# Optimization experiments

Hardware: AMD Instinct MI355X
Metric: run time of the kernel (lower is better)

Reference implementation:

```python
import jax, jax.numpy as jnp
import numpy as np

WIN = 64
SHIFT = 32
HEADS = 12


def setup_inputs() -> dict:
    key = jax.random.key(0)
    ks = jax.random.split(key, 6)
    D = 768
    return {
        'x': jax.random.normal(ks[0], (16, 4096, D), dtype=jnp.float32),
        'qkv_w': jax.random.normal(ks[1], (3 * D, D), dtype=jnp.float32) * (D ** -0.5),
        'qkv_b': jax.random.normal(ks[2], (3 * D,), dtype=jnp.float32) * 0.02,
        'proj_w': jax.random.normal(ks[3], (D, D), dtype=jnp.float32) * (D ** -0.5),
        'proj_b': jax.random.normal(ks[4], (D,), dtype=jnp.float32) * 0.02,
        'rel_bias': jax.random.normal(ks[5], (HEADS, 2 * WIN - 1), dtype=jnp.float32) * 0.02,
    }


def reference(x, qkv_w, qkv_b, proj_w, proj_b, rel_bias):
    B, N, D = x.shape
    H, hd = HEADS, D // HEADS
    scale = hd ** -0.5
    if SHIFT:
        x = jnp.roll(x, SHIFT, axis=1)
    pad = (-N) % WIN
    if pad:
        x = jnp.pad(x, ((0, 0), (0, pad), (0, 0)))
    Np = x.shape[1]
    nW = Np // WIN
    # [B*nW, w, D] windows
    xw = x.reshape(B * nW, WIN, D)
    qkv = xw @ qkv_w.T + qkv_b                       # [B*nW, w, 3D]
    qkv = qkv.reshape(B * nW, WIN, 3, H, hd).transpose(2, 0, 3, 1, 4)
    q, k, v = qkv[0], qkv[1], qkv[2]                 # [B*nW, H, w, hd]
    attn = jnp.einsum('bhqd,bhkd->bhqk', q, k) * scale
    idx = jnp.arange(WIN)
    rel = idx[None, :] - idx[:, None] + (WIN - 1)    # [w, w] in [0, 2w-2]
    attn = attn + rel_bias[:, rel][None]             # gather bias per head
    attn = jax.nn.softmax(attn, axis=-1)
    y = jnp.einsum('bhqk,bhkd->bhqd', attn, v)       # [B*nW, H, w, hd]
    y = y.transpose(0, 2, 1, 3).reshape(B * nW, WIN, D)
    y = y @ proj_w.T + proj_b
    y = y.reshape(B, Np, D)
    if pad:
        y = y[:, :N, :]
    if SHIFT:
        y = jnp.roll(y, -SHIFT, axis=1)
    return y
```

## Files before the change

kernel.cpp:

```cpp
#include <hip/hip_runtime.h>
#include <hip/hip_bf16.h>
#include <stdint.h>

#define SEQ     4096
#define NBATCH  16
#define DMODEL  768
#define NHEAD   12
#define HDIM    64
#define WINSZ   64
#define SHIFT_T 32
#define QKV_N   (3*DMODEL)

typedef __attribute__((ext_vector_type(8)))  short bf16x8;
typedef __attribute__((ext_vector_type(4)))  float f32x4;

static __device__ __forceinline__ unsigned short f2bf(float f) {
  union { float f; unsigned u; } v; v.f = f;
  unsigned r = v.u + 0x7fffu + ((v.u >> 16) & 1u);
  return (unsigned short)(r >> 16);
}

#define G2L(gp, lp) __builtin_amdgcn_global_load_lds( \
    (const __attribute__((address_space(1))) unsigned*)(const void*)(gp), \
    (__attribute__((address_space(3))) unsigned*)(void*)(lp), 16, 0, 0)

__global__ void k_cvt_x(const float* __restrict__ x, unsigned short* __restrict__ xb,
                        long long c0, long long n8) {
  for (long long i = (long long)blockIdx.x*blockDim.x + threadIdx.x; i < n8;
       i += (long long)gridDim.x*blockDim.x) {
    long long e = i*8;
    int d = (int)(e % DMODEL);
    long long gt = c0 + e / DMODEL;
    int t = (int)(gt & (SEQ-1));
    long long b = gt >> 12;
    int ts = (t - SHIFT_T) & (SEQ-1);
    const float* src = x + (((b << 12) + ts) * (long long)DMODEL + d);
    float4 a0 = *(const float4*)src;
    float4 a1 = *(const float4*)(src + 4);
    bf16x8 o;
    o[0]=(short)f2bf(a0.x); o[1]=(short)f2bf(a0.y); o[2]=(short)f2bf(a0.z); o[3]=(short)f2bf(a0.w);
    o[4]=(short)f2bf(a1.x); o[5]=(short)f2bf(a1.y); o[6]=(short)f2bf(a1.z); o[7]=(short)f2bf(a1.w);
    *(bf16x8*)(xb + e) = o;
  }
}

__global__ void k_cvt_w(const float* __restrict__ w, unsigned short* __restrict__ wb, int n8) {
  int i = blockIdx.x*blockDim.x + threadIdx.x;
  if (i >= n8) return;
  float4 a0 = ((const float4*)w)[2*i];
  float4 a1 = ((const float4*)w)[2*i+1];
  bf16x8 o;
  o[0]=(short)f2bf(a0.x); o[1]=(short)f2bf(a0.y); o[2]=(short)f2bf(a0.z); o[3]=(short)f2bf(a0.w);
  o[4]=(short)f2bf(a1.x); o[5]=(short)f2bf(a1.y); o[6]=(short)f2bf(a1.z); o[7]=(short)f2bf(a1.w);
  ((bf16x8*)wb)[i] = o;
}

#define MFMA16(a,b,c) __builtin_amdgcn_mfma_f32_16x16x32_bf16(a,b,c,0,0,0)
#define LDS8(p) (*(const bf16x8*)(p))

template<int MODE>
__global__ __launch_bounds__(512, 1)
void k_gemm256(const unsigned short* __restrict__ A, const unsigned short* __restrict__ Bw,
               const float* __restrict__ bias, unsigned short* __restrict__ Cb,
               float* __restrict__ Cf, int M, int N, int K, int nTN, long long c0) {
  __shared__ char lds[131072];
  const int nt = K >> 6;
  int nwg = gridDim.x;
  int cpx = nwg >> 3;
  int wg  = (blockIdx.x & 7) * cpx + (blockIdx.x >> 3);
  int bm = wg / nTN, bn = wg - bm*nTN;
  long long m0 = (long long)bm * 256;
  int n0 = bn * 256;
  int tid = threadIdx.x;
  int lane = tid & 63, wid = tid >> 6;
  int wr = wid >> 2, wc = wid & 3;
  int cl = lane & 15, g4 = lane >> 4;

  const long long K2 = 2LL * K;
  int L  = tid * 16;
  int Ls = L ^ (((L >> 7) & 7) << 4);
  int srow = Ls >> 7, scol = Ls & 127;
  const char* gAr0 = (const char*)A + (m0 +       srow) * K2 + scol;
  const char* gAr1 = (const char*)A + (m0 +  64 + srow) * K2 + scol;
  const char* gAr2 = (const char*)A + (m0 + 128 + srow) * K2 + scol;
  const char* gAr3 = (const char*)A + (m0 + 192 + srow) * K2 + scol;
  const char* gBr0 = (const char*)Bw + (long long)(n0 +       srow) * K2 + scol;
  const char* gBr1 = (const char*)Bw + (long long)(n0 +  64 + srow) * K2 + scol;
  const char* gBr2 = (const char*)Bw + (long long)(n0 + 128 + srow) * K2 + scol;
  const char* gBr3 = (const char*)Bw + (long long)(n0 + 192 + srow) * K2 + scol;

  int p0 = cl*128 + ((g4*16) ^ ((cl & 7) << 4));
  int p1 = p0 ^ 64;
  int RA0 = wr*16384;
  int RA1 = wr*16384 + 8192;
  int BB  = 32768 + wc*8192;

  f32x4 acc[8][4];
  #pragma unroll
  for (int i = 0; i < 8; ++i)
    #pragma unroll
    for (int j = 0; j < 4; ++j) acc[i][j] = (f32x4){0.f,0.f,0.f,0.f};

#define MMPH(MA, MB, x0, x1, y0, y1) \
  acc[MA][0]=MFMA16(x0,b00,acc[MA][0]); acc[MA][1]=MFMA16(x0,b10,acc[MA][1]); \
  acc[MA][2]=MFMA16(x0,b20,acc[MA][2]); acc[MA][3]=MFMA16(x0,b30,acc[MA][3]); \
  acc[MB][0]=MFMA16(y0,b00,acc[MB][0]); acc[MB][1]=MFMA16(y0,b10,acc[MB][1]); \
  acc[MB][2]=MFMA16(y0,b20,acc[MB][2]); acc[MB][3]=MFMA16(y0,b30,acc[MB][3]); \
  acc[MA][0]=MFMA16(x1,b01,acc[MA][0]); acc[MA][1]=MFMA16(x1,b11,acc[MA][1]); \
  acc[MA][2]=MFMA16(x1,b21,acc[MA][2]); acc[MA][3]=MFMA16(x1,b31,acc[MA][3]); \
  acc[MB][0]=MFMA16(y1,b01,acc[MB][0]); acc[MB][1]=MFMA16(y1,b11,acc[MB][1]); \
  acc[MB][2]=MFMA16(y1,b21,acc[MB][2]); acc[MB][3]=MFMA16(y1,b31,acc[MB][3]);

#define BARR __builtin_amdgcn_s_barrier()
#define SBAR __builtin_amdgcn_sched_barrier(0)
#define LGK0 do { asm volatile("s_waitcnt lgkmcnt(0)" ::: "memory"); SBAR; } while(0)

#define TILE(RD, ST, DOSTAGE, WBSTR, DOWA) do {                               \
    const char* rb = (RD); char* stb = (ST);                                  \
    bf16x8 b00,b01,b10,b11,b20,b21,b30,b31;                                   \
    {                              \
      bf16x8 x0 = LDS8(rb + RA0        + p0), x1 = LDS8(rb + RA0        + p1);\
      bf16x8 y0 = LDS8(rb + RA0 + 2048 + p0), y1 = LDS8(rb + RA0 + 2048 + p1);\
      b00 = LDS8(rb + BB        + p0);  b01 = LDS8(rb + BB        + p1);      \
      b10 = LDS8(rb + BB + 2048 + p0);  b11 = LDS8(rb + BB + 2048 + p1);      \
      b20 = LDS8(rb + BB + 4096 + p0);  b21 = LDS8(rb + BB + 4096 + p1);      \
      b30 = LDS8(rb + BB + 6144 + p0);  b31 = LDS8(rb + BB + 6144 + p1);      \
      if (DOSTAGE) { G2L(gBr0, stb + 32768 + L); G2L(gBr1, stb + 40960 + L); }\
      asm volatile("s_waitcnt lgkmcnt(8)" ::: "memory"); SBAR;                \
      BARR; LGK0;                                                             \
      __builtin_amdgcn_s_setprio(1);                                          \
      MMPH(0, 1, x0, x1, y0, y1)                                              \
      __builtin_amdgcn_s_setprio(0); SBAR; BARR;                              \
    }                                                                         \
    {              \
      bf16x8 x0 = LDS8(rb + RA0 + 4096 + p0), x1 = LDS8(rb + RA0 + 4096 + p1);\
      bf16x8 y0 = LDS8(rb + RA0 + 6144 + p0), y1 = LDS8(rb + RA0 + 6144 + p1);\
      if (DOSTAGE) { G2L(gBr2, stb + 49152 + L); G2L(gBr3, stb + 57344 + L); }\
      SBAR; BARR; LGK0;                                                       \
      __builtin_amdgcn_s_setprio(1);                                          \
      MMPH(2, 3, x0, x1, y0, y1)                                              \
      __builtin_amdgcn_s_setprio(0); SBAR;                                    \
      asm volatile(WBSTR ::: "memory"); SBAR; BARR;                           \
    }                                                                         \
    {                                      \
      bf16x8 x0 = LDS8(rb + RA1        + p0), x1 = LDS8(rb + RA1        + p1);\
      bf16x8 y0 = LDS8(rb + RA1 + 2048 + p0), y1 = LDS8(rb + RA1 + 2048 + p1);\
      if (DOSTAGE) { G2L(gAr0, stb + L); G2L(gAr2, stb + 16384 + L); }        \
      SBAR; BARR; LGK0;                                                       \
      __builtin_amdgcn_s_setprio(1);                                          \
      MMPH(4, 5, x0, x1, y0, y1)                                              \
      __builtin_amdgcn_s_setprio(0); SBAR; BARR;                              \
    }                                                                         \
    {        \
      bf16x8 x0 = LDS8(rb + RA1 + 4096 + p0), x1 = LDS8(rb + RA1 + 4096 + p1);\
      bf16x8 y0 = LDS8(rb + RA1 + 6144 + p0), y1 = LDS8(rb + RA1 + 6144 + p1);\
      if (DOSTAGE) { G2L(gAr1, stb + 8192 + L); G2L(gAr3, stb + 24576 + L);   \
                     gAr0 += 128; gAr1 += 128; gAr2 += 128; gAr3 += 128;      \
                     gBr0 += 128; gBr1 += 128; gBr2 += 128; gBr3 += 128; }    \
      SBAR; BARR; LGK0;                                                       \
      __builtin_amdgcn_s_setprio(1);                                          \
      MMPH(6, 7, x0, x1, y0, y1)                                              \
      __builtin_amdgcn_s_setprio(0); SBAR;                                    \
      if (DOWA) { asm volatile("s_waitcnt vmcnt(2)" ::: "memory"); }          \
      SBAR; BARR;                                                             \
    }                                                                         \
  } while (0)

  G2L(gBr0, lds + 32768 + L); G2L(gBr1, lds + 40960 + L);
  G2L(gBr2, lds + 49152 + L); G2L(gBr3, lds + 57344 + L);
  G2L(gAr0, lds + L);         G2L(gAr2, lds + 16384 + L);
  G2L(gAr1, lds + 8192 + L);  G2L(gAr3, lds + 24576 + L);
  gAr0 += 128; gAr1 += 128; gAr2 += 128; gAr3 += 128;
  gBr0 += 128; gBr1 += 128; gBr2 += 128; gBr3 += 128;
  asm volatile("s_waitcnt vmcnt(2)" ::: "memory");
  SBAR; BARR;

  char* const bufA = lds;
  char* const bufB = lds + 65536;
  for (int i = 0; i < (nt - 2) / 2; ++i) {
    TILE(bufA, bufB, 1, "s_waitcnt vmcnt(4)", 1);
    TILE(bufB, bufA, 1, "s_waitcnt vmcnt(4)", 1);
  }
  TILE(bufA, bufB, 1, "s_waitcnt vmcnt(4)", 1);
  TILE(bufB, bufA, 0, "s_waitcnt vmcnt(0)", 0);
#undef TILE
#undef MMPH

  #pragma unroll
  for (int mf = 0; mf < 8; ++mf) {
    #pragma unroll
    for (int nf = 0; nf < 4; ++nf) {
      int n = n0 + wc*64 + nf*16 + cl;
      float bv = bias[n];
      #pragma unroll
      for (int r = 0; r < 4; ++r) {
        long long m = m0 + wr*128 + mf*16 + g4*4 + r;
        float v = acc[mf][nf][r] + bv;
        if (MODE == 0) {
          Cb[m * (long long)N + n] = f2bf(v);
        } else {
          long long gm = c0 + m;
          long long om = (gm & ~(long long)(SEQ-1)) | ((gm - SHIFT_T) & (long long)(SEQ-1));
          Cf[om * (long long)N + n] = v;
        }
      }
    }
  }
}

__global__ __launch_bounds__(256, 4)
void k_attn(const unsigned short* __restrict__ qkv, const float* __restrict__ rel_bias,
            unsigned short* __restrict__ y) {
  int w = blockIdx.x / NHEAD;
  int h = blockIdx.x - w*NHEAD;
  __shared__ unsigned short sQ[64*72], sK[64*72], sV[64*72];
  __shared__ unsigned short sP[4][16*72];
  __shared__ float rb[128];
  int tid = threadIdx.x, lane = tid & 63, wid = tid >> 6;
  int cl = lane & 15, g4 = lane >> 4;

  if (tid < 2*WINSZ - 1) rb[tid] = rel_bias[h*(2*WINSZ-1) + tid];

  const unsigned short* base = qkv + (long long)w*WINSZ*QKV_N + h*HDIM;
  #pragma unroll
  for (int pass = 0; pass < 2; ++pass) {
    int row = (tid >> 3) + pass*32;
    int ch  = tid & 7;
    const unsigned short* src = base + (long long)row*QKV_N + ch*8;
    *(bf16x8*)(sQ + row*72 + ch*8) = *(const bf16x8*)(src);
    *(bf16x8*)(sK + row*72 + ch*8) = *(const bf16x8*)(src + DMODEL);
    *(bf16x8*)(sV + row*72 + ch*8) = *(const bf16x8*)(src + 2*DMODEL);
  }
  __syncthreads();

  f32x4 sc[4];
  #pragma unroll
  for (int nt = 0; nt < 4; ++nt) sc[nt] = (f32x4){0.f,0.f,0.f,0.f};
  #pragma unroll
  for (int kk = 0; kk < 2; ++kk) {
    bf16x8 aq = *(const bf16x8*)(sQ + (wid*16 + cl)*72 + kk*32 + g4*8);
    #pragma unroll
    for (int nt = 0; nt < 4; ++nt) {
      bf16x8 bk = *(const bf16x8*)(sK + (nt*16 + cl)*72 + kk*32 + g4*8);
      sc[nt] = __builtin_amdgcn_mfma_f32_16x16x32_bf16(aq, bk, sc[nt], 0, 0, 0);
    }
  }

  float pv[4][4];
  #pragma unroll
  for (int r = 0; r < 4; ++r) {
    int qi = wid*16 + g4*4 + r;
    float mx = -1e30f;
    #pragma unroll
    for (int nt = 0; nt < 4; ++nt) {
      int kj = nt*16 + cl;
      float v = sc[nt][r]*0.125f + rb[kj - qi + (WINSZ-1)];
      pv[nt][r] = v;
      mx = fmaxf(mx, v);
    }
    #pragma unroll
    for (int m = 1; m < 16; m <<= 1) mx = fmaxf(mx, __shfl_xor(mx, m, 64));
    float sum = 0.f;
    #pragma unroll
    for (int nt = 0; nt < 4; ++nt) { float e = __expf(pv[nt][r]-mx); pv[nt][r] = e; sum += e; }
    #pragma unroll
    for (int m = 1; m < 16; m <<= 1) sum += __shfl_xor(sum, m, 64);
    float inv = 1.f / sum;
    #pragma unroll
    for (int nt = 0; nt < 4; ++nt)
      sP[wid][(g4*4+r)*72 + nt*16 + cl] = f2bf(pv[nt][r]*inv);
  }

  f32x4 o[4];
  #pragma unroll
  for (int nt = 0; nt < 4; ++nt) o[nt] = (f32x4){0.f,0.f,0.f,0.f};
  #pragma unroll
  for (int kk = 0; kk < 2; ++kk) {
    bf16x8 ap = *(const bf16x8*)(&sP[wid][cl*72 + kk*32 + g4*8]);
    #pragma unroll
    for (int nt = 0; nt < 4; ++nt) {
      bf16x8 bv;
      #pragma unroll
      for (int j = 0; j < 8; ++j)
        bv[j] = (short)sV[(kk*32 + g4*8 + j)*72 + nt*16 + cl];
      o[nt] = __builtin_amdgcn_mfma_f32_16x16x32_bf16(ap, bv, o[nt], 0, 0, 0);
    }
  }

  long long tokbase = (long long)w * WINSZ;
  #pragma unroll
  for (int nt = 0; nt < 4; ++nt)
    #pragma unroll
    for (int r = 0; r < 4; ++r) {
      int row = wid*16 + g4*4 + r;
      y[(tokbase + row) * (long long)DMODEL + h*HDIM + nt*16 + cl] = f2bf(o[nt][r]);
    }
}

extern "C" void kernel_launch(void* const* d_in, const int* in_sizes, int n_in,
                              void* d_out, int out_size, void* d_ws, size_t ws_size,
                              hipStream_t stream) {
  const float* x      = (const float*)d_in[0];
  const float* qkv_w  = (const float*)d_in[1];
  const float* qkv_b  = (const float*)d_in[2];
  const float* proj_w = (const float*)d_in[3];
  const float* proj_b = (const float*)d_in[4];
  const float* rel_b  = (const float*)d_in[5];
  float* out = (float*)d_out;

  const long long NTOK = (long long)NBATCH * SEQ;
  const size_t wbytes = (size_t)QKV_N*DMODEL*2 + (size_t)DMODEL*DMODEL*2;

  int C = 16;
  for (int c : {1, 2, 4, 8, 16}) {
    size_t tpc = (size_t)NTOK / c;
    size_t need = tpc*QKV_N*2 + tpc*DMODEL*2 + wbytes;
    if (need <= ws_size) { C = c; break; }
  }
  long long tpc = NTOK / C;

  char* ws = (char*)d_ws;
  unsigned short* qkvb = (unsigned short*)ws;
  unsigned short* xb   = (unsigned short*)(ws + (size_t)tpc*QKV_N*2);
  unsigned short* wq   = (unsigned short*)(ws + (size_t)tpc*QKV_N*2 + (size_t)tpc*DMODEL*2);
  unsigned short* wp   = wq + (size_t)QKV_N*DMODEL;

  k_cvt_w<<<(QKV_N*DMODEL/8 + 255)/256, 256, 0, stream>>>(qkv_w, wq, QKV_N*DMODEL/8);
  k_cvt_w<<<(DMODEL*DMODEL/8 + 255)/256, 256, 0, stream>>>(proj_w, wp, DMODEL*DMODEL/8);

  for (int c = 0; c < C; ++c) {
    long long c0 = (long long)c * tpc;
    long long n8 = tpc * DMODEL / 8;
    int cvtGrid = (int)((n8 + 255) / 256); if (cvtGrid > 2048) cvtGrid = 2048;
    k_cvt_x<<<cvtGrid, 256, 0, stream>>>(x, xb, c0, n8);

    int mT = (int)(tpc / 256);
    k_gemm256<0><<<mT * (QKV_N/256), 512, 0, stream>>>(xb, wq, qkv_b, qkvb, nullptr,
                                                       (int)tpc, QKV_N, DMODEL, QKV_N/256, c0);
    k_attn<<<(int)(tpc/WINSZ) * NHEAD, 256, 0, stream>>>(qkvb, rel_b, xb );
    k_gemm256<1><<<mT * (DMODEL/256), 512, 0, stream>>>(xb, wp, proj_b, nullptr, out,
                                                        (int)tpc, DMODEL, DMODEL, DMODEL/256, c0);
  }
}
```

Measured before the change: 503.3 us.

## Fuse x conversion, QKV projection and window attention into one kernel

```diff
diff --git a/kernel.cpp b/kernel.cpp
--- a/kernel.cpp
+++ b/kernel.cpp
@@ -24,25 +24,8 @@
     (const __attribute__((address_space(1))) unsigned*)(const void*)(gp), \
     (__attribute__((address_space(3))) unsigned*)(void*)(lp), 16, 0, 0)
 
-__global__ void k_cvt_x(const float* __restrict__ x, unsigned short* __restrict__ xb,
-                        long long c0, long long n8) {
-  for (long long i = (long long)blockIdx.x*blockDim.x + threadIdx.x; i < n8;
-       i += (long long)gridDim.x*blockDim.x) {
-    long long e = i*8;
-    int d = (int)(e % DMODEL);
-    long long gt = c0 + e / DMODEL;
-    int t = (int)(gt & (SEQ-1));
-    long long b = gt >> 12;
-    int ts = (t - SHIFT_T) & (SEQ-1);
-    const float* src = x + (((b << 12) + ts) * (long long)DMODEL + d);
-    float4 a0 = *(const float4*)src;
-    float4 a1 = *(const float4*)(src + 4);
-    bf16x8 o;
-    o[0]=(short)f2bf(a0.x); o[1]=(short)f2bf(a0.y); o[2]=(short)f2bf(a0.z); o[3]=(short)f2bf(a0.w);
-    o[4]=(short)f2bf(a1.x); o[5]=(short)f2bf(a1.y); o[6]=(short)f2bf(a1.z); o[7]=(short)f2bf(a1.w);
-    *(bf16x8*)(xb + e) = o;
-  }
-}
+#define MFMA16(a,b,c) __builtin_amdgcn_mfma_f32_16x16x32_bf16(a,b,c,0,0,0)
+#define LDS8(p) (*(const bf16x8*)(p))
 
 __global__ void k_cvt_w(const float* __restrict__ w, unsigned short* __restrict__ wb, int n8) {
   int i = blockIdx.x*blockDim.x + threadIdx.x;
@@ -55,8 +38,177 @@
   ((bf16x8*)wb)[i] = o;
 }
 
-#define MFMA16(a,b,c) __builtin_amdgcn_mfma_f32_16x16x32_bf16(a,b,c,0,0,0)
-#define LDS8(p) (*(const bf16x8*)(p))
+__global__ __launch_bounds__(512, 4)
+void k_qkv_attn(const float* __restrict__ x, const unsigned short* __restrict__ wqkv,
+                const float* __restrict__ qkv_b, const float* __restrict__ rel_bias,
+                unsigned short* __restrict__ y) {
+  __shared__ char ldsA[16384];
+  __shared__ char ldsS[55296];
+  __shared__ float rb[128];
+  int blk = blockIdx.x;
+  int tid = threadIdx.x, lane = tid & 63, wid = tid >> 6;
+  int cl = lane & 15, g4 = lane >> 4;
+  int wr = wid >> 2, wc = wid & 3;
+
+  int arow = tid >> 2, ac4 = tid & 3;
+  long long gt = (long long)blk*128 + arow;
+  long long bb = gt >> 12;
+  int ts = ((int)(gt & (SEQ-1)) - SHIFT_T) & (SEQ-1);
+  const float* xsrc = x + ((bb << 12) + ts) * (long long)DMODEL + ac4*16;
+  int akey = (arow & 7) << 4;
+  int awb0 = arow*128 + ((ac4*32)      ^ akey);
+  int awb1 = arow*128 + ((ac4*32 + 16) ^ akey);
+
+  int L  = tid * 16;
+  int Ls = L ^ (((L >> 7) & 7) << 4);
+  int srow = Ls >> 7, scol = Ls & 127;
+
+  int key = (cl & 7) << 4;
+  int am  = (wr*64 + cl) * 128;
+  int ch0 = (g4*16) ^ key;
+  int ch1 = ch0 ^ 64;
+  int bn  = (wc*16 + cl) * 128;
+
+  const long long BROW = 2LL * DMODEL;
+  unsigned short* sQKV = (unsigned short*)ldsS;
+
+  for (int h = 0; h < NHEAD; ++h) {
+    const char* gB0 = (const char*)wqkv + (h*64 + srow) * BROW + scol;
+    const char* gB1 = gB0 + 768 * BROW;
+    const char* gB2 = gB1 + 768 * BROW;
+
+    f32x4 acc[4][3];
+    #pragma unroll
+    for (int i = 0; i < 4; ++i)
+      #pragma unroll
+      for (int j = 0; j < 3; ++j) acc[i][j] = (f32x4){0.f,0.f,0.f,0.f};
+
+    for (int kt = 0; kt < 12; ++kt) {
+      __syncthreads();
+      const float* xs = xsrc + kt*64;
+      float4 f0 = *(const float4*)xs;
+      float4 f1 = *(const float4*)(xs + 4);
+      float4 f2 = *(const float4*)(xs + 8);
+      float4 f3 = *(const float4*)(xs + 12);
+      bf16x8 v0, v1;
+      v0[0]=(short)f2bf(f0.x); v0[1]=(short)f2bf(f0.y); v0[2]=(short)f2bf(f0.z); v0[3]=(short)f2bf(f0.w);
+      v0[4]=(short)f2bf(f1.x); v0[5]=(short)f2bf(f1.y); v0[6]=(short)f2bf(f1.z); v0[7]=(short)f2bf(f1.w);
+      v1[0]=(short)f2bf(f2.x); v1[1]=(short)f2bf(f2.y); v1[2]=(short)f2bf(f2.z); v1[3]=(short)f2bf(f2.w);
+      v1[4]=(short)f2bf(f3.x); v1[5]=(short)f2bf(f3.y); v1[6]=(short)f2bf(f3.z); v1[7]=(short)f2bf(f3.w);
+      *(bf16x8*)(ldsA + awb0) = v0;
+      *(bf16x8*)(ldsA + awb1) = v1;
+      G2L(gB0 + kt*128, ldsS + L);
+      G2L(gB1 + kt*128, ldsS + 8192 + L);
+      G2L(gB2 + kt*128, ldsS + 16384 + L);
+      __syncthreads();
+      bf16x8 a0[4], a1[4], b0[3], b1[3];
+      #pragma unroll
+      for (int mr = 0; mr < 4; ++mr) {
+        a0[mr] = LDS8(ldsA + am + mr*2048 + ch0);
+        a1[mr] = LDS8(ldsA + am + mr*2048 + ch1);
+      }
+      #pragma unroll
+      for (int nf = 0; nf < 3; ++nf) {
+        b0[nf] = LDS8(ldsS + nf*8192 + bn + ch0);
+        b1[nf] = LDS8(ldsS + nf*8192 + bn + ch1);
+      }
+      #pragma unroll
+      for (int mr = 0; mr < 4; ++mr)
+        #pragma unroll
+        for (int nf = 0; nf < 3; ++nf) {
+          acc[mr][nf] = MFMA16(a0[mr], b0[nf], acc[mr][nf]);
+          acc[mr][nf] = MFMA16(a1[mr], b1[nf], acc[mr][nf]);
+        }
+    }
+    __syncthreads();
+    #pragma unroll
+    for (int nf = 0; nf < 3; ++nf) {
+      float bv = qkv_b[nf*768 + h*64 + wc*16 + cl];
+      #pragma unroll
+      for (int mr = 0; mr < 4; ++mr)
+        #pragma unroll
+        for (int r = 0; r < 4; ++r) {
+          int row = wr*64 + mr*16 + g4*4 + r;
+          sQKV[nf*9216 + row*72 + wc*16 + cl] = f2bf(acc[mr][nf][r] + bv);
+        }
+    }
+    if (tid < 2*WINSZ - 1) rb[tid] = rel_bias[h*(2*WINSZ-1) + tid];
+    __syncthreads();
+
+    {
+      int wl = wid >> 2, ww = wid & 3;
+      unsigned short* sQ = sQKV +          wl*64*72;
+      unsigned short* sK = sQKV +  9216 + wl*64*72;
+      unsigned short* sV = sQKV + 18432 + wl*64*72;
+      char* sPb = ldsA + wid*2048;
+
+      f32x4 sc[4];
+      #pragma unroll
+      for (int nt = 0; nt < 4; ++nt) sc[nt] = (f32x4){0.f,0.f,0.f,0.f};
+      #pragma unroll
+      for (int kk = 0; kk < 2; ++kk) {
+        bf16x8 aq = LDS8(sQ + (ww*16 + cl)*72 + kk*32 + g4*8);
+        #pragma unroll
+        for (int nt = 0; nt < 4; ++nt) {
+          bf16x8 bk = LDS8(sK + (nt*16 + cl)*72 + kk*32 + g4*8);
+          sc[nt] = MFMA16(aq, bk, sc[nt]);
+        }
+      }
+
+      float pv[4][4];
+      #pragma unroll
+      for (int r = 0; r < 4; ++r) {
+        int qi = ww*16 + g4*4 + r;
+        float mx = -1e30f;
+        #pragma unroll
+        for (int nt = 0; nt < 4; ++nt) {
+          int kj = nt*16 + cl;
+          float v = sc[nt][r]*0.125f + rb[kj - qi + (WINSZ-1)];
+          pv[nt][r] = v;
+          mx = fmaxf(mx, v);
+        }
+        #pragma unroll
+        for (int m = 1; m < 16; m <<= 1) mx = fmaxf(mx, __shfl_xor(mx, m, 64));
+        float sum = 0.f;
+        #pragma unroll
+        for (int nt = 0; nt < 4; ++nt) { float e = __expf(pv[nt][r]-mx); pv[nt][r] = e; sum += e; }
+        #pragma unroll
+        for (int m = 1; m < 16; m <<= 1) sum += __shfl_xor(sum, m, 64);
+        float inv = 1.f / sum;
+        int prow = g4*4 + r;
+        int pkey = (prow & 7) << 4;
+        #pragma unroll
+        for (int nt = 0; nt < 4; ++nt)
+          *(unsigned short*)(sPb + prow*128 + (((nt*16 + cl)*2) ^ pkey)) = f2bf(pv[nt][r]*inv);
+      }
+
+      f32x4 o[4];
+      #pragma unroll
+      for (int nt = 0; nt < 4; ++nt) o[nt] = (f32x4){0.f,0.f,0.f,0.f};
+      #pragma unroll
+      for (int kk = 0; kk < 2; ++kk) {
+        bf16x8 ap = LDS8(sPb + cl*128 + ((kk*64 + g4*16) ^ ((cl & 7) << 4)));
+        #pragma unroll
+        for (int nt = 0; nt < 4; ++nt) {
+          bf16x8 bv;
+          #pragma unroll
+          for (int j = 0; j < 8; ++j)
+            bv[j] = (short)sV[(kk*32 + g4*8 + j)*72 + nt*16 + cl];
+          o[nt] = MFMA16(ap, bv, o[nt]);
+        }
+      }
+
+      long long tokbase = (long long)blk * 128;
+      #pragma unroll
+      for (int nt = 0; nt < 4; ++nt)
+        #pragma unroll
+        for (int r = 0; r < 4; ++r) {
+          int row = wid*16 + g4*4 + r;
+          y[(tokbase + row) * (long long)DMODEL + h*HDIM + nt*16 + cl] = f2bf(o[nt][r]);
+        }
+    }
+  }
+}
 
 template<int MODE>
 __global__ __launch_bounds__(512, 1)
@@ -116,15 +268,15 @@
 #define LGK0 do { asm volatile("s_waitcnt lgkmcnt(0)" ::: "memory"); SBAR; } while(0)
 
 #define TILE(RD, ST, DOSTAGE, WBSTR, DOWA) do {                               \
-    const char* rb = (RD); char* stb = (ST);                                  \
+    const char* rbuf = (RD); char* stb = (ST);                                \
     bf16x8 b00,b01,b10,b11,b20,b21,b30,b31;                                   \
-    {                              \
-      bf16x8 x0 = LDS8(rb + RA0        + p0), x1 = LDS8(rb + RA0        + p1);\
-      bf16x8 y0 = LDS8(rb + RA0 + 2048 + p0), y1 = LDS8(rb + RA0 + 2048 + p1);\
-      b00 = LDS8(rb + BB        + p0);  b01 = LDS8(rb + BB        + p1);      \
-      b10 = LDS8(rb + BB + 2048 + p0);  b11 = LDS8(rb + BB + 2048 + p1);      \
-      b20 = LDS8(rb + BB + 4096 + p0);  b21 = LDS8(rb + BB + 4096 + p1);      \
-      b30 = LDS8(rb + BB + 6144 + p0);  b31 = LDS8(rb + BB + 6144 + p1);      \
+    {                                                            \
+      bf16x8 x0 = LDS8(rbuf + RA0        + p0), x1 = LDS8(rbuf + RA0        + p1);\
+      bf16x8 y0 = LDS8(rbuf + RA0 + 2048 + p0), y1 = LDS8(rbuf + RA0 + 2048 + p1);\
+      b00 = LDS8(rbuf + BB        + p0);  b01 = LDS8(rbuf + BB        + p1);  \
+      b10 = LDS8(rbuf + BB + 2048 + p0);  b11 = LDS8(rbuf + BB + 2048 + p1);  \
+      b20 = LDS8(rbuf + BB + 4096 + p0);  b21 = LDS8(rbuf + BB + 4096 + p1);  \
+      b30 = LDS8(rbuf + BB + 6144 + p0);  b31 = LDS8(rbuf + BB + 6144 + p1);  \
       if (DOSTAGE) { G2L(gBr0, stb + 32768 + L); G2L(gBr1, stb + 40960 + L); }\
       asm volatile("s_waitcnt lgkmcnt(8)" ::: "memory"); SBAR;                \
       BARR; LGK0;                                                             \
@@ -132,9 +284,9 @@
       MMPH(0, 1, x0, x1, y0, y1)                                              \
       __builtin_amdgcn_s_setprio(0); SBAR; BARR;                              \
     }                                                                         \
-    {              \
-      bf16x8 x0 = LDS8(rb + RA0 + 4096 + p0), x1 = LDS8(rb + RA0 + 4096 + p1);\
-      bf16x8 y0 = LDS8(rb + RA0 + 6144 + p0), y1 = LDS8(rb + RA0 + 6144 + p1);\
+    {                                                            \
+      bf16x8 x0 = LDS8(rbuf + RA0 + 4096 + p0), x1 = LDS8(rbuf + RA0 + 4096 + p1);\
+      bf16x8 y0 = LDS8(rbuf + RA0 + 6144 + p0), y1 = LDS8(rbuf + RA0 + 6144 + p1);\
       if (DOSTAGE) { G2L(gBr2, stb + 49152 + L); G2L(gBr3, stb + 57344 + L); }\
       SBAR; BARR; LGK0;                                                       \
       __builtin_amdgcn_s_setprio(1);                                          \
@@ -142,18 +294,18 @@
       __builtin_amdgcn_s_setprio(0); SBAR;                                    \
       asm volatile(WBSTR ::: "memory"); SBAR; BARR;                           \
     }                                                                         \
-    {                                      \
-      bf16x8 x0 = LDS8(rb + RA1        + p0), x1 = LDS8(rb + RA1        + p1);\
-      bf16x8 y0 = LDS8(rb + RA1 + 2048 + p0), y1 = LDS8(rb + RA1 + 2048 + p1);\
+    {                                                            \
+      bf16x8 x0 = LDS8(rbuf + RA1        + p0), x1 = LDS8(rbuf + RA1        + p1);\
+      bf16x8 y0 = LDS8(rbuf + RA1 + 2048 + p0), y1 = LDS8(rbuf + RA1 + 2048 + p1);\
       if (DOSTAGE) { G2L(gAr0, stb + L); G2L(gAr2, stb + 16384 + L); }        \
       SBAR; BARR; LGK0;                                                       \
       __builtin_amdgcn_s_setprio(1);                                          \
       MMPH(4, 5, x0, x1, y0, y1)                                              \
       __builtin_amdgcn_s_setprio(0); SBAR; BARR;                              \
     }                                                                         \
-    {        \
-      bf16x8 x0 = LDS8(rb + RA1 + 4096 + p0), x1 = LDS8(rb + RA1 + 4096 + p1);\
-      bf16x8 y0 = LDS8(rb + RA1 + 6144 + p0), y1 = LDS8(rb + RA1 + 6144 + p1);\
+    {                                                            \
+      bf16x8 x0 = LDS8(rbuf + RA1 + 4096 + p0), x1 = LDS8(rbuf + RA1 + 4096 + p1);\
+      bf16x8 y0 = LDS8(rbuf + RA1 + 6144 + p0), y1 = LDS8(rbuf + RA1 + 6144 + p1);\
       if (DOSTAGE) { G2L(gAr1, stb + 8192 + L); G2L(gAr3, stb + 24576 + L);   \
                      gAr0 += 128; gAr1 += 128; gAr2 += 128; gAr3 += 128;      \
                      gBr0 += 128; gBr1 += 128; gBr2 += 128; gBr3 += 128; }    \
@@ -208,95 +360,6 @@
   }
 }
 
-__global__ __launch_bounds__(256, 4)
-void k_attn(const unsigned short* __restrict__ qkv, const float* __restrict__ rel_bias,
-            unsigned short* __restrict__ y) {
-  int w = blockIdx.x / NHEAD;
-  int h = blockIdx.x - w*NHEAD;
-  __shared__ unsigned short sQ[64*72], sK[64*72], sV[64*72];
-  __shared__ unsigned short sP[4][16*72];
-  __shared__ float rb[128];
-  int tid = threadIdx.x, lane = tid & 63, wid = tid >> 6;
-  int cl = lane & 15, g4 = lane >> 4;
-
-  if (tid < 2*WINSZ - 1) rb[tid] = rel_bias[h*(2*WINSZ-1) + tid];
-
-  const unsigned short* base = qkv + (long long)w*WINSZ*QKV_N + h*HDIM;
-  #pragma unroll
-  for (int pass = 0; pass < 2; ++pass) {
-    int row = (tid >> 3) + pass*32;
-    int ch  = tid & 7;
-    const unsigned short* src = base + (long long)row*QKV_N + ch*8;
-    *(bf16x8*)(sQ + row*72 + ch*8) = *(const bf16x8*)(src);
-    *(bf16x8*)(sK + row*72 + ch*8) = *(const bf16x8*)(src + DMODEL);
-    *(bf16x8*)(sV + row*72 + ch*8) = *(const bf16x8*)(src + 2*DMODEL);
-  }
-  __syncthreads();
-
-  f32x4 sc[4];
-  #pragma unroll
-  for (int nt = 0; nt < 4; ++nt) sc[nt] = (f32x4){0.f,0.f,0.f,0.f};
-  #pragma unroll
-  for (int kk = 0; kk < 2; ++kk) {
-    bf16x8 aq = *(const bf16x8*)(sQ + (wid*16 + cl)*72 + kk*32 + g4*8);
-    #pragma unroll
-    for (int nt = 0; nt < 4; ++nt) {
-      bf16x8 bk = *(const bf16x8*)(sK + (nt*16 + cl)*72 + kk*32 + g4*8);
-      sc[nt] = __builtin_amdgcn_mfma_f32_16x16x32_bf16(aq, bk, sc[nt], 0, 0, 0);
-    }
-  }
-
-  float pv[4][4];
-  #pragma unroll
-  for (int r = 0; r < 4; ++r) {
-    int qi = wid*16 + g4*4 + r;
-    float mx = -1e30f;
-    #pragma unroll
-    for (int nt = 0; nt < 4; ++nt) {
-      int kj = nt*16 + cl;
-      float v = sc[nt][r]*0.125f + rb[kj - qi + (WINSZ-1)];
-      pv[nt][r] = v;
-      mx = fmaxf(mx, v);
-    }
-    #pragma unroll
-    for (int m = 1; m < 16; m <<= 1) mx = fmaxf(mx, __shfl_xor(mx, m, 64));
-    float sum = 0.f;
-    #pragma unroll
-    for (int nt = 0; nt < 4; ++nt) { float e = __expf(pv[nt][r]-mx); pv[nt][r] = e; sum += e; }
-    #pragma unroll
-    for (int m = 1; m < 16; m <<= 1) sum += __shfl_xor(sum, m, 64);
-    float inv = 1.f / sum;
-    #pragma unroll
-    for (int nt = 0; nt < 4; ++nt)
-      sP[wid][(g4*4+r)*72 + nt*16 + cl] = f2bf(pv[nt][r]*inv);
-  }
-
-  f32x4 o[4];
-  #pragma unroll
-  for (int nt = 0; nt < 4; ++nt) o[nt] = (f32x4){0.f,0.f,0.f,0.f};
-  #pragma unroll
-  for (int kk = 0; kk < 2; ++kk) {
-    bf16x8 ap = *(const bf16x8*)(&sP[wid][cl*72 + kk*32 + g4*8]);
-    #pragma unroll
-    for (int nt = 0; nt < 4; ++nt) {
-      bf16x8 bv;
-      #pragma unroll
-      for (int j = 0; j < 8; ++j)
-        bv[j] = (short)sV[(kk*32 + g4*8 + j)*72 + nt*16 + cl];
-      o[nt] = __builtin_amdgcn_mfma_f32_16x16x32_bf16(ap, bv, o[nt], 0, 0, 0);
-    }
-  }
-
-  long long tokbase = (long long)w * WINSZ;
-  #pragma unroll
-  for (int nt = 0; nt < 4; ++nt)
-    #pragma unroll
-    for (int r = 0; r < 4; ++r) {
-      int row = wid*16 + g4*4 + r;
-      y[(tokbase + row) * (long long)DMODEL + h*HDIM + nt*16 + cl] = f2bf(o[nt][r]);
-    }
-}
-
 extern "C" void kernel_launch(void* const* d_in, const int* in_sizes, int n_in,
                               void* d_out, int out_size, void* d_ws, size_t ws_size,
                               hipStream_t stream) {
@@ -309,36 +372,18 @@
   float* out = (float*)d_out;
 
   const long long NTOK = (long long)NBATCH * SEQ;
-  const size_t wbytes = (size_t)QKV_N*DMODEL*2 + (size_t)DMODEL*DMODEL*2;
-
-  int C = 16;
-  for (int c : {1, 2, 4, 8, 16}) {
-    size_t tpc = (size_t)NTOK / c;
-    size_t need = tpc*QKV_N*2 + tpc*DMODEL*2 + wbytes;
-    if (need <= ws_size) { C = c; break; }
-  }
-  long long tpc = NTOK / C;
 
   char* ws = (char*)d_ws;
-  unsigned short* qkvb = (unsigned short*)ws;
-  unsigned short* xb   = (unsigned short*)(ws + (size_t)tpc*QKV_N*2);
-  unsigned short* wq   = (unsigned short*)(ws + (size_t)tpc*QKV_N*2 + (size_t)tpc*DMODEL*2);
-  unsigned short* wp   = wq + (size_t)QKV_N*DMODEL;
+  unsigned short* xb = (unsigned short*)ws;
+  unsigned short* wq = (unsigned short*)(ws + (size_t)NTOK*DMODEL*2);
+  unsigned short* wp = wq + (size_t)QKV_N*DMODEL;
 
   k_cvt_w<<<(QKV_N*DMODEL/8 + 255)/256, 256, 0, stream>>>(qkv_w, wq, QKV_N*DMODEL/8);
   k_cvt_w<<<(DMODEL*DMODEL/8 + 255)/256, 256, 0, stream>>>(proj_w, wp, DMODEL*DMODEL/8);
 
-  for (int c = 0; c < C; ++c) {
-    long long c0 = (long long)c * tpc;
-    long long n8 = tpc * DMODEL / 8;
-    int cvtGrid = (int)((n8 + 255) / 256); if (cvtGrid > 2048) cvtGrid = 2048;
-    k_cvt_x<<<cvtGrid, 256, 0, stream>>>(x, xb, c0, n8);
-
-    int mT = (int)(tpc / 256);
-    k_gemm256<0><<<mT * (QKV_N/256), 512, 0, stream>>>(xb, wq, qkv_b, qkvb, nullptr,
-                                                       (int)tpc, QKV_N, DMODEL, QKV_N/256, c0);
-    k_attn<<<(int)(tpc/WINSZ) * NHEAD, 256, 0, stream>>>(qkvb, rel_b, xb );
-    k_gemm256<1><<<mT * (DMODEL/256), 512, 0, stream>>>(xb, wp, proj_b, nullptr, out,
-                                                        (int)tpc, DMODEL, DMODEL, DMODEL/256, c0);
-  }
-}
+  k_qkv_attn<<<(int)(NTOK/128), 512, 0, stream>>>(x, wq, qkv_b, rel_b, xb);
+
+  int mT = (int)(NTOK / 256);
+  k_gemm256<1><<<mT * (DMODEL/256), 512, 0, stream>>>(xb, wp, proj_b, nullptr, out,
+                                                      (int)NTOK, DMODEL, DMODEL, DMODEL/256, 0);
+}
```

Result: slower. 574.2 us (+14.1%).

## Fuse fp32-to-bf16 conversion and roll of x into QKV GEMM A-load

Applied to the files above, without the earlier changes.

```diff
diff --git a/kernel.cpp b/kernel.cpp
--- a/kernel.cpp
+++ b/kernel.cpp
@@ -20,29 +20,27 @@
   return (unsigned short)(r >> 16);
 }
 
+static __device__ __forceinline__ unsigned cvtpk(float lo, float hi) {
+  unsigned r;
+  asm("v_cvt_pk_bf16_f32 %0, %1, %2" : "=v"(r) : "v"(lo), "v"(hi));
+  return r;
+}
+static __device__ __forceinline__ bf16x8 pk8(float4 a, float4 b) {
+  union { unsigned u[4]; bf16x8 v; } t;
+  t.u[0] = cvtpk(a.x, a.y); t.u[1] = cvtpk(a.z, a.w);
+  t.u[2] = cvtpk(b.x, b.y); t.u[3] = cvtpk(b.z, b.w);
+  return t.v;
+}
+
 #define G2L(gp, lp) __builtin_amdgcn_global_load_lds( \
     (const __attribute__((address_space(1))) unsigned*)(const void*)(gp), \
     (__attribute__((address_space(3))) unsigned*)(void*)(lp), 16, 0, 0)
 
-__global__ void k_cvt_x(const float* __restrict__ x, unsigned short* __restrict__ xb,
-                        long long c0, long long n8) {
-  for (long long i = (long long)blockIdx.x*blockDim.x + threadIdx.x; i < n8;
-       i += (long long)gridDim.x*blockDim.x) {
-    long long e = i*8;
-    int d = (int)(e % DMODEL);
-    long long gt = c0 + e / DMODEL;
-    int t = (int)(gt & (SEQ-1));
-    long long b = gt >> 12;
-    int ts = (t - SHIFT_T) & (SEQ-1);
-    const float* src = x + (((b << 12) + ts) * (long long)DMODEL + d);
-    float4 a0 = *(const float4*)src;
-    float4 a1 = *(const float4*)(src + 4);
-    bf16x8 o;
-    o[0]=(short)f2bf(a0.x); o[1]=(short)f2bf(a0.y); o[2]=(short)f2bf(a0.z); o[3]=(short)f2bf(a0.w);
-    o[4]=(short)f2bf(a1.x); o[5]=(short)f2bf(a1.y); o[6]=(short)f2bf(a1.z); o[7]=(short)f2bf(a1.w);
-    *(bf16x8*)(xb + e) = o;
-  }
-}
+#define MFMA16(a,b,c) __builtin_amdgcn_mfma_f32_16x16x32_bf16(a,b,c,0,0,0)
+#define LDS8(p) (*(const bf16x8*)(p))
+#define BARR __builtin_amdgcn_s_barrier()
+#define SBAR __builtin_amdgcn_sched_barrier(0)
+#define LGK0 do { asm volatile("s_waitcnt lgkmcnt(0)" ::: "memory"); SBAR; } while(0)
 
 __global__ void k_cvt_w(const float* __restrict__ w, unsigned short* __restrict__ wb, int n8) {
   int i = blockIdx.x*blockDim.x + threadIdx.x;
@@ -55,8 +53,174 @@
   ((bf16x8*)wb)[i] = o;
 }
 
-#define MFMA16(a,b,c) __builtin_amdgcn_mfma_f32_16x16x32_bf16(a,b,c,0,0,0)
-#define LDS8(p) (*(const bf16x8*)(p))
+__global__ __launch_bounds__(512, 1)
+void k_qkvgemm(const float* __restrict__ x, const unsigned short* __restrict__ Bw,
+               const float* __restrict__ bias, unsigned short* __restrict__ Cb,
+               int M, long long c0) {
+  __shared__ char lds[131072];
+  const int nt = DMODEL >> 6;
+  const int nTN = QKV_N / 256;
+  int nwg = gridDim.x;
+  int cpx = nwg >> 3;
+  int wg  = (blockIdx.x & 7) * cpx + (blockIdx.x >> 3);
+  int bm = wg / nTN, bn = wg - bm*nTN;
+  long long m0 = (long long)bm * 256;
+  int n0 = bn * 256;
+  int tid = threadIdx.x;
+  int lane = tid & 63, wid = tid >> 6;
+  int wr = wid >> 2, wc = wid & 3;
+  int cl = lane & 15, g4 = lane >> 4;
+
+  int arr = tid >> 3, ac = tid & 7;
+  int awL = arr*128 + ((ac*16) ^ ((arr & 7) << 4));
+  const char *ap0, *ap1, *ap2, *ap3;
+  {
+    long long gt0 = c0 + m0 + arr;
+    long long gt1 = gt0 + 64, gt2 = gt0 + 128, gt3 = gt0 + 192;
+#define ROLLP(gt) ((const char*)(x + (((gt >> 12) << 12) + ((((int)(gt & (SEQ-1))) - SHIFT_T) & (SEQ-1))) * (long long)DMODEL + ac*8))
+    ap0 = ROLLP(gt0); ap1 = ROLLP(gt1); ap2 = ROLLP(gt2); ap3 = ROLLP(gt3);
+#undef ROLLP
+  }
+
+  const long long K2 = 2LL * DMODEL;
+  int L  = tid * 16;
+  int Ls = L ^ (((L >> 7) & 7) << 4);
+  int srow = Ls >> 7, scol = Ls & 127;
+  const char* gBr0 = (const char*)Bw + (long long)(n0 +       srow) * K2 + scol;
+  const char* gBr1 = (const char*)Bw + (long long)(n0 +  64 + srow) * K2 + scol;
+  const char* gBr2 = (const char*)Bw + (long long)(n0 + 128 + srow) * K2 + scol;
+  const char* gBr3 = (const char*)Bw + (long long)(n0 + 192 + srow) * K2 + scol;
+
+  int p0 = cl*128 + ((g4*16) ^ ((cl & 7) << 4));
+  int p1 = p0 ^ 64;
+  int RA0 = wr*16384;
+  int RA1 = wr*16384 + 8192;
+  int BB  = 32768 + wc*8192;
+
+  f32x4 acc[8][4];
+  #pragma unroll
+  for (int i = 0; i < 8; ++i)
+    #pragma unroll
+    for (int j = 0; j < 4; ++j) acc[i][j] = (f32x4){0.f,0.f,0.f,0.f};
+
+#define QMM(MA, MB, x0, x1, y0, y1) \
+  acc[MA][0]=MFMA16(x0,b00,acc[MA][0]); acc[MA][1]=MFMA16(x0,b10,acc[MA][1]); \
+  acc[MA][2]=MFMA16(x0,b20,acc[MA][2]); acc[MA][3]=MFMA16(x0,b30,acc[MA][3]); \
+  acc[MB][0]=MFMA16(y0,b00,acc[MB][0]); acc[MB][1]=MFMA16(y0,b10,acc[MB][1]); \
+  acc[MB][2]=MFMA16(y0,b20,acc[MB][2]); acc[MB][3]=MFMA16(y0,b30,acc[MB][3]); \
+  acc[MA][0]=MFMA16(x1,b01,acc[MA][0]); acc[MA][1]=MFMA16(x1,b11,acc[MA][1]); \
+  acc[MA][2]=MFMA16(x1,b21,acc[MA][2]); acc[MA][3]=MFMA16(x1,b31,acc[MA][3]); \
+  acc[MB][0]=MFMA16(y1,b01,acc[MB][0]); acc[MB][1]=MFMA16(y1,b11,acc[MB][1]); \
+  acc[MB][2]=MFMA16(y1,b21,acc[MB][2]); acc[MB][3]=MFMA16(y1,b31,acc[MB][3]);
+
+#define STW(DST) do {                                                         \
+    *(bf16x8*)((DST) +         awL) = pk8(fa0, fb0);                          \
+    *(bf16x8*)((DST) +  8192 + awL) = pk8(fa1, fb1);                          \
+    *(bf16x8*)((DST) + 16384 + awL) = pk8(fa2, fb2);                          \
+    *(bf16x8*)((DST) + 24576 + awL) = pk8(fa3, fb3);                          \
+  } while (0)
+
+#define QTILE(RD, ST, DOSTAGE) do {                                           \
+    const char* rbuf = (RD); char* stb = (ST);                                \
+    bf16x8 b00,b01,b10,b11,b20,b21,b30,b31;                                   \
+    float4 fa0,fb0,fa1,fb1,fa2,fb2,fa3,fb3;                                   \
+    {          \
+      bf16x8 x0 = LDS8(rbuf + RA0        + p0), x1 = LDS8(rbuf + RA0        + p1);\
+      bf16x8 y0 = LDS8(rbuf + RA0 + 2048 + p0), y1 = LDS8(rbuf + RA0 + 2048 + p1);\
+      b00 = LDS8(rbuf + BB        + p0);  b01 = LDS8(rbuf + BB        + p1);  \
+      b10 = LDS8(rbuf + BB + 2048 + p0);  b11 = LDS8(rbuf + BB + 2048 + p1);  \
+      b20 = LDS8(rbuf + BB + 4096 + p0);  b21 = LDS8(rbuf + BB + 4096 + p1);  \
+      b30 = LDS8(rbuf + BB + 6144 + p0);  b31 = LDS8(rbuf + BB + 6144 + p1);  \
+      if (DOSTAGE) {                                                          \
+        fa0 = *(const float4*)ap0; fb0 = *(const float4*)(ap0 + 16);          \
+        fa1 = *(const float4*)ap1; fb1 = *(const float4*)(ap1 + 16);          \
+        fa2 = *(const float4*)ap2; fb2 = *(const float4*)(ap2 + 16);          \
+        fa3 = *(const float4*)ap3; fb3 = *(const float4*)(ap3 + 16);          \
+      }                                                                       \
+      asm volatile("s_waitcnt lgkmcnt(8)" ::: "memory"); SBAR;                \
+      BARR; LGK0;                                                             \
+      __builtin_amdgcn_s_setprio(1);                                          \
+      QMM(0, 1, x0, x1, y0, y1)                                               \
+      __builtin_amdgcn_s_setprio(0); SBAR; BARR;                              \
+    }                                                                         \
+    {                    \
+      bf16x8 x0 = LDS8(rbuf + RA0 + 4096 + p0), x1 = LDS8(rbuf + RA0 + 4096 + p1);\
+      bf16x8 y0 = LDS8(rbuf + RA0 + 6144 + p0), y1 = LDS8(rbuf + RA0 + 6144 + p1);\
+      if (DOSTAGE) { G2L(gBr0, stb + 32768 + L); G2L(gBr1, stb + 40960 + L);  \
+                     G2L(gBr2, stb + 49152 + L); G2L(gBr3, stb + 57344 + L); }\
+      SBAR; BARR; LGK0;                                                       \
+      __builtin_amdgcn_s_setprio(1);                                          \
+      QMM(2, 3, x0, x1, y0, y1)                                               \
+      __builtin_amdgcn_s_setprio(0); SBAR;                                    \
+      if (DOSTAGE) { asm volatile("s_waitcnt vmcnt(4)" ::: "memory"); }       \
+      SBAR; BARR;                                                             \
+    }                                                                         \
+    {            \
+      bf16x8 x0 = LDS8(rbuf + RA1        + p0), x1 = LDS8(rbuf + RA1        + p1);\
+      bf16x8 y0 = LDS8(rbuf + RA1 + 2048 + p0), y1 = LDS8(rbuf + RA1 + 2048 + p1);\
+      SBAR; BARR; LGK0;                                                       \
+      __builtin_amdgcn_s_setprio(1);                                          \
+      QMM(4, 5, x0, x1, y0, y1)                                               \
+      __builtin_amdgcn_s_setprio(0); SBAR;                                    \
+      if (DOSTAGE) { STW(stb); }                                              \
+      SBAR; BARR;                                                             \
+    }                                                                         \
+    {      \
+      bf16x8 x0 = LDS8(rbuf + RA1 + 4096 + p0), x1 = LDS8(rbuf + RA1 + 4096 + p1);\
+      bf16x8 y0 = LDS8(rbuf + RA1 + 6144 + p0), y1 = LDS8(rbuf + RA1 + 6144 + p1);\
+      SBAR; BARR; LGK0;                                                       \
+      __builtin_amdgcn_s_setprio(1);                                          \
+      QMM(6, 7, x0, x1, y0, y1)                                               \
+      __builtin_amdgcn_s_setprio(0); SBAR;                                    \
+      if (DOSTAGE) { ap0 += 256; ap1 += 256; ap2 += 256; ap3 += 256;          \
+                     gBr0 += 128; gBr1 += 128; gBr2 += 128; gBr3 += 128;      \
+                     asm volatile("s_waitcnt vmcnt(0)" ::: "memory"); }       \
+      SBAR; BARR;                                                             \
+    }                                                                         \
+  } while (0)
+
+  {
+    float4 fa0 = *(const float4*)ap0, fb0 = *(const float4*)(ap0 + 16);
+    float4 fa1 = *(const float4*)ap1, fb1 = *(const float4*)(ap1 + 16);
+    float4 fa2 = *(const float4*)ap2, fb2 = *(const float4*)(ap2 + 16);
+    float4 fa3 = *(const float4*)ap3, fb3 = *(const float4*)(ap3 + 16);
+    G2L(gBr0, lds + 32768 + L); G2L(gBr1, lds + 40960 + L);
+    G2L(gBr2, lds + 49152 + L); G2L(gBr3, lds + 57344 + L);
+    asm volatile("s_waitcnt vmcnt(4)" ::: "memory"); SBAR;
+    STW(lds);
+    ap0 += 256; ap1 += 256; ap2 += 256; ap3 += 256;
+    gBr0 += 128; gBr1 += 128; gBr2 += 128; gBr3 += 128;
+    asm volatile("s_waitcnt vmcnt(0)" ::: "memory");
+    asm volatile("s_waitcnt lgkmcnt(0)" ::: "memory");
+    SBAR; BARR;
+  }
+
+  char* const bufA = lds;
+  char* const bufB = lds + 65536;
+  for (int i = 0; i < (nt - 2) / 2; ++i) {
+    QTILE(bufA, bufB, 1);
+    QTILE(bufB, bufA, 1);
+  }
+  QTILE(bufA, bufB, 1);
+  QTILE(bufB, bufA, 0);
+#undef QTILE
+#undef QMM
+#undef STW
+
+  #pragma unroll
+  for (int mf = 0; mf < 8; ++mf) {
+    #pragma unroll
+    for (int nf = 0; nf < 4; ++nf) {
+      int n = n0 + wc*64 + nf*16 + cl;
+      float bv = bias[n];
+      #pragma unroll
+      for (int r = 0; r < 4; ++r) {
+        long long m = m0 + wr*128 + mf*16 + g4*4 + r;
+        Cb[m * (long long)QKV_N + n] = f2bf(acc[mf][nf][r] + bv);
+      }
+    }
+  }
+}
 
 template<int MODE>
 __global__ __launch_bounds__(512, 1)
@@ -111,20 +275,15 @@
   acc[MB][0]=MFMA16(y1,b01,acc[MB][0]); acc[MB][1]=MFMA16(y1,b11,acc[MB][1]); \
   acc[MB][2]=MFMA16(y1,b21,acc[MB][2]); acc[MB][3]=MFMA16(y1,b31,acc[MB][3]);
 
-#define BARR __builtin_amdgcn_s_barrier()
-#define SBAR __builtin_amdgcn_sched_barrier(0)
-#define LGK0 do { asm volatile("s_waitcnt lgkmcnt(0)" ::: "memory"); SBAR; } while(0)
-
 #define TILE(RD, ST, DOSTAGE, WBSTR, DOWA) do {                               \
-    const char* rb = (RD); char* stb = (ST);                                  \
+    const char* rbuf = (RD); char* stb = (ST);                                \
     bf16x8 b00,b01,b10,b11,b20,b21,b30,b31;                                   \
-    {                              \
-      bf16x8 x0 = LDS8(rb + RA0        + p0), x1 = LDS8(rb + RA0        + p1);\
-      bf16x8 y0 = LDS8(rb + RA0 + 2048 + p0), y1 = LDS8(rb + RA0 + 2048 + p1);\
-      b00 = LDS8(rb + BB        + p0);  b01 = LDS8(rb + BB        + p1);      \
-      b10 = LDS8(rb + BB + 2048 + p0);  b11 = LDS8(rb + BB + 2048 + p1);      \
-      b20 = LDS8(rb + BB + 4096 + p0);  b21 = LDS8(rb + BB + 4096 + p1);      \
-      b30 = LDS8(rb + BB + 6144 + p0);  b31 = LDS8(rb + BB + 6144 + p1);      \
+    { bf16x8 x0 = LDS8(rbuf + RA0        + p0), x1 = LDS8(rbuf + RA0        + p1);\
+      bf16x8 y0 = LDS8(rbuf + RA0 + 2048 + p0), y1 = LDS8(rbuf + RA0 + 2048 + p1);\
+      b00 = LDS8(rbuf + BB        + p0);  b01 = LDS8(rbuf + BB        + p1);  \
+      b10 = LDS8(rbuf + BB + 2048 + p0);  b11 = LDS8(rbuf + BB + 2048 + p1);  \
+      b20 = LDS8(rbuf + BB + 4096 + p0);  b21 = LDS8(rbuf + BB + 4096 + p1);  \
+      b30 = LDS8(rbuf + BB + 6144 + p0);  b31 = LDS8(rbuf + BB + 6144 + p1);  \
       if (DOSTAGE) { G2L(gBr0, stb + 32768 + L); G2L(gBr1, stb + 40960 + L); }\
       asm volatile("s_waitcnt lgkmcnt(8)" ::: "memory"); SBAR;                \
       BARR; LGK0;                                                             \
@@ -132,9 +291,8 @@
       MMPH(0, 1, x0, x1, y0, y1)                                              \
       __builtin_amdgcn_s_setprio(0); SBAR; BARR;                              \
     }                                                                         \
-    {              \
-      bf16x8 x0 = LDS8(rb + RA0 + 4096 + p0), x1 = LDS8(rb + RA0 + 4096 + p1);\
-      bf16x8 y0 = LDS8(rb + RA0 + 6144 + p0), y1 = LDS8(rb + RA0 + 6144 + p1);\
+    { bf16x8 x0 = LDS8(rbuf + RA0 + 4096 + p0), x1 = LDS8(rbuf + RA0 + 4096 + p1);\
+      bf16x8 y0 = LDS8(rbuf + RA0 + 6144 + p0), y1 = LDS8(rbuf + RA0 + 6144 + p1);\
       if (DOSTAGE) { G2L(gBr2, stb + 49152 + L); G2L(gBr3, stb + 57344 + L); }\
       SBAR; BARR; LGK0;                                                       \
       __builtin_amdgcn_s_setprio(1);                                          \
@@ -142,18 +300,16 @@
       __builtin_amdgcn_s_setprio(0); SBAR;                                    \
       asm volatile(WBSTR ::: "memory"); SBAR; BARR;                           \
     }                                                                         \
-    {                                      \
-      bf16x8 x0 = LDS8(rb + RA1        + p0), x1 = LDS8(rb + RA1        + p1);\
-      bf16x8 y0 = LDS8(rb + RA1 + 2048 + p0), y1 = LDS8(rb + RA1 + 2048 + p1);\
+    { bf16x8 x0 = LDS8(rbuf + RA1        + p0), x1 = LDS8(rbuf + RA1        + p1);\
+      bf16x8 y0 = LDS8(rbuf + RA1 + 2048 + p0), y1 = LDS8(rbuf + RA1 + 2048 + p1);\
       if (DOSTAGE) { G2L(gAr0, stb + L); G2L(gAr2, stb + 16384 + L); }        \
       SBAR; BARR; LGK0;                                                       \
       __builtin_amdgcn_s_setprio(1);                                          \
       MMPH(4, 5, x0, x1, y0, y1)                                              \
       __builtin_amdgcn_s_setprio(0); SBAR; BARR;                              \
     }                                                                         \
-    {        \
-      bf16x8 x0 = LDS8(rb + RA1 + 4096 + p0), x1 = LDS8(rb + RA1 + 4096 + p1);\
-      bf16x8 y0 = LDS8(rb + RA1 + 6144 + p0), y1 = LDS8(rb + RA1 + 6144 + p1);\
+    { bf16x8 x0 = LDS8(rbuf + RA1 + 4096 + p0), x1 = LDS8(rbuf + RA1 + 4096 + p1);\
+      bf16x8 y0 = LDS8(rbuf + RA1 + 6144 + p0), y1 = LDS8(rbuf + RA1 + 6144 + p1);\
       if (DOSTAGE) { G2L(gAr1, stb + 8192 + L); G2L(gAr3, stb + 24576 + L);   \
                      gAr0 += 128; gAr1 += 128; gAr2 += 128; gAr3 += 128;      \
                      gBr0 += 128; gBr1 += 128; gBr2 += 128; gBr3 += 128; }    \
@@ -242,7 +398,7 @@
     #pragma unroll
     for (int nt = 0; nt < 4; ++nt) {
       bf16x8 bk = *(const bf16x8*)(sK + (nt*16 + cl)*72 + kk*32 + g4*8);
-      sc[nt] = __builtin_amdgcn_mfma_f32_16x16x32_bf16(aq, bk, sc[nt], 0, 0, 0);
+      sc[nt] = MFMA16(aq, bk, sc[nt]);
     }
   }
 
@@ -283,7 +439,7 @@
       #pragma unroll
       for (int j = 0; j < 8; ++j)
         bv[j] = (short)sV[(kk*32 + g4*8 + j)*72 + nt*16 + cl];
-      o[nt] = __builtin_amdgcn_mfma_f32_16x16x32_bf16(ap, bv, o[nt], 0, 0, 0);
+      o[nt] = MFMA16(ap, bv, o[nt]);
     }
   }
 
@@ -312,7 +468,7 @@
   const size_t wbytes = (size_t)QKV_N*DMODEL*2 + (size_t)DMODEL*DMODEL*2;
 
   int C = 16;
-  for (int c : {1, 2, 4, 8, 16}) {
+  for (int c : {2, 4, 8, 16}) {
     size_t tpc = (size_t)NTOK / c;
     size_t need = tpc*QKV_N*2 + tpc*DMODEL*2 + wbytes;
     if (need <= ws_size) { C = c; break; }
@@ -321,7 +477,7 @@
 
   char* ws = (char*)d_ws;
   unsigned short* qkvb = (unsigned short*)ws;
-  unsigned short* xb   = (unsigned short*)(ws + (size_t)tpc*QKV_N*2);
+  unsigned short* yb   = (unsigned short*)(ws + (size_t)tpc*QKV_N*2);
   unsigned short* wq   = (unsigned short*)(ws + (size_t)tpc*QKV_N*2 + (size_t)tpc*DMODEL*2);
   unsigned short* wp   = wq + (size_t)QKV_N*DMODEL;
 
@@ -330,15 +486,10 @@
 
   for (int c = 0; c < C; ++c) {
     long long c0 = (long long)c * tpc;
-    long long n8 = tpc * DMODEL / 8;
-    int cvtGrid = (int)((n8 + 255) / 256); if (cvtGrid > 2048) cvtGrid = 2048;
-    k_cvt_x<<<cvtGrid, 256, 0, stream>>>(x, xb, c0, n8);
-
     int mT = (int)(tpc / 256);
-    k_gemm256<0><<<mT * (QKV_N/256), 512, 0, stream>>>(xb, wq, qkv_b, qkvb, nullptr,
-                                                       (int)tpc, QKV_N, DMODEL, QKV_N/256, c0);
-    k_attn<<<(int)(tpc/WINSZ) * NHEAD, 256, 0, stream>>>(qkvb, rel_b, xb );
-    k_gemm256<1><<<mT * (DMODEL/256), 512, 0, stream>>>(xb, wp, proj_b, nullptr, out,
+    k_qkvgemm<<<mT * (QKV_N/256), 512, 0, stream>>>(x, wq, qkv_b, qkvb, (int)tpc, c0);
+    k_attn<<<(int)(tpc/WINSZ) * NHEAD, 256, 0, stream>>>(qkvb, rel_b, yb);
+    k_gemm256<1><<<mT * (DMODEL/256), 512, 0, stream>>>(yb, wp, proj_b, nullptr, out,
                                                         (int)tpc, DMODEL, DMODEL, DMODEL/256, c0);
   }
 }
```

Result: slower. 551.3 us (+9.5%).
